# Kernel tuning notes

Measured on AMD Instinct MI355X. Metric: run time of the kernel, lower is better.

The kernel has to match this reference:

```python
import jax, jax.numpy as jnp
import numpy as np

H = 8          # query heads
HKV = 4        # kv heads
D = 256        # head dim
GROUPS = H // HKV
HIDDEN = 2304
WINDOW = 2048  # sliding window
SOFTCAP = 50.0
SCALE = (HIDDEN // H) ** -0.5  # query_pre_attn_scalar uses hidden//heads, not head_dim
NEG = -1e9
ROPE_BASE = 10000.0


def _rope_tables(L, offset=0, dtype=jnp.float32):
    inv_freq = 1.0 / (ROPE_BASE ** (jnp.arange(0, D, 2, dtype=jnp.float32) / D))
    t = jnp.arange(offset, offset + L, dtype=jnp.float32)
    freqs = jnp.outer(t, inv_freq)                    # [L, D/2]
    emb = jnp.concatenate([freqs, freqs], axis=-1)    # [L, D]
    return jnp.cos(emb).astype(dtype), jnp.sin(emb).astype(dtype)


def _rotate_half(x):
    x1, x2 = jnp.split(x, 2, axis=-1)
    return jnp.concatenate([-x2, x1], axis=-1)


def _apply_rope(x, cos, sin):
    # x: [B, h, L, D]; cos/sin: [L, D]
    return x * cos[None, None] + _rotate_half(x) * sin[None, None]


def setup_inputs() -> dict:
    key = jax.random.key(0)
    ks = jax.random.split(key, 5)
    B, L = 1, 4096
    x = jax.random.normal(ks[0], (B, L, HIDDEN), dtype=jnp.float32)
    wq = jax.random.normal(ks[1], (HIDDEN, H * D), dtype=jnp.float32) * 0.02
    wk = jax.random.normal(ks[2], (HIDDEN, HKV * D), dtype=jnp.float32) * 0.02
    wv = jax.random.normal(ks[3], (HIDDEN, HKV * D), dtype=jnp.float32) * 0.02
    wo = jax.random.normal(ks[4], (H * D, HIDDEN), dtype=jnp.float32) * 0.02
    # additive causal mask [1,1,L,L]
    causal = jnp.triu(jnp.full((L, L), NEG, dtype=jnp.float32), k=1)
    mask = causal[None, None]
    return {"x": x, "mask": mask, "wq": wq, "wk": wk, "wv": wv, "wo": wo}


def reference(x, mask, wq, wk, wv, wo):
    B, L, _ = x.shape
    q = (x @ wq).reshape(B, L, H, D).transpose(0, 2, 1, 3)     # [B,H,L,D]
    k = (x @ wk).reshape(B, L, HKV, D).transpose(0, 2, 1, 3)   # [B,HKV,L,D]
    v = (x @ wv).reshape(B, L, HKV, D).transpose(0, 2, 1, 3)

    cos, sin = _rope_tables(L, 0, q.dtype)
    q = _apply_rope(q, cos, sin)
    k = _apply_rope(k, cos, sin)

    # GQA: repeat_interleave kv heads
    k = jnp.repeat(k, GROUPS, axis=1)  # [B,H,L,D]
    v = jnp.repeat(v, GROUPS, axis=1)

    attn = jnp.einsum("bhqd,bhkd->bhqk", q, k) * SCALE
    attn = SOFTCAP * jnp.tanh(attn / SOFTCAP)
    attn = attn + mask

    kv_len = attn.shape[-1]
    if kv_len > WINDOW:  # sliding branch: keep only last WINDOW key columns
        col_keep = jnp.arange(kv_len) >= (kv_len - WINDOW)  # [kv_len]
        attn = jnp.where(col_keep[None, None, None, :], attn, NEG)

    attn = jax.nn.softmax(attn.astype(jnp.float32), axis=-1).astype(q.dtype)
    out = jnp.einsum("bhqk,bhkd->bhqd", attn, v)
    out = out.transpose(0, 2, 1, 3).reshape(B, L, H * D)
    return out @ wo
```

## Files before the change

kernel.cpp:

```cpp
#include <hip/hip_runtime.h>

typedef unsigned short u16;
typedef __bf16 bf16x8 __attribute__((ext_vector_type(8)));
typedef float floatx4 __attribute__((ext_vector_type(4)));
typedef unsigned short u16x4 __attribute__((ext_vector_type(4)));
typedef unsigned short u16x8 __attribute__((ext_vector_type(8)));

#define L_SEQ 4096
#define HID   2304
#define NH    8
#define NKV   4
#define HD    256
#define QDIM  2048
#define KVDIM 1024
#define SCALE_F 0.05892556509887896f

__device__ __forceinline__ u16 f2bf(float f) {
  unsigned u = __float_as_uint(f);
  u += 0x7FFFu + ((u >> 16) & 1u);
  return (u16)(u >> 16);
}
__device__ __forceinline__ float bf2f(u16 h) {
  return __uint_as_float(((unsigned)h) << 16);
}

__device__ __forceinline__ void async_load16(const u16* g, u16* lds_base) {
  __builtin_amdgcn_global_load_lds(
      (const __attribute__((address_space(1))) unsigned int*)g,
      (__attribute__((address_space(3))) unsigned int*)lds_base, 16, 0, 0);
}

__device__ __forceinline__ int swz(int m) { return (m + (m >> 2)) & 3; }

__global__ __launch_bounds__(256)
void cast_kernel(const float* __restrict__ in, u16* __restrict__ out, int n4) {
  int i = blockIdx.x * 256 + threadIdx.x;
  if (i < n4) {
    float4 v = *reinterpret_cast<const float4*>(&in[(size_t)i * 4]);
    u16x4 o;
    o[0] = f2bf(v.x); o[1] = f2bf(v.y); o[2] = f2bf(v.z); o[3] = f2bf(v.w);
    *reinterpret_cast<u16x4*>(&out[(size_t)i * 4]) = o;
  }
}

__global__ __launch_bounds__(256)
void transpose_kernel(const float* __restrict__ wq, const float* __restrict__ wk,
                      const float* __restrict__ wv, const float* __restrict__ wo,
                      u16* __restrict__ wqkvT, u16* __restrict__ woT) {
  const int z = blockIdx.z;
  const float* W; u16* WT; int K, N;
  if (z == 0)      { W = wq; WT = wqkvT;                            K = HID;  N = QDIM; }
  else if (z == 1) { W = wk; WT = wqkvT + (size_t)QDIM * HID;       K = HID;  N = KVDIM; }
  else if (z == 2) { W = wv; WT = wqkvT + (size_t)(QDIM + KVDIM) * HID; K = HID; N = KVDIM; }
  else             { W = wo; WT = woT;                              K = QDIM; N = HID; }
  const int n0 = blockIdx.x * 32, k0 = blockIdx.y * 32;
  if (n0 >= N || k0 >= K) return;
  __shared__ u16 t[32][33];
  const int c = threadIdx.x & 31, r4 = (threadIdx.x >> 5) * 4;
#pragma unroll
  for (int i = 0; i < 4; ++i)
    t[r4 + i][c] = f2bf(W[(size_t)(k0 + r4 + i) * N + n0 + c]);
  __syncthreads();
#pragma unroll
  for (int i = 0; i < 4; ++i)
    WT[(size_t)(n0 + r4 + i) * K + k0 + c] = t[c][r4 + i];
}

#define G256_NT 36

#define G256_BARRIER() __builtin_amdgcn_s_barrier()

#define G256_STAGE(bb, X, kh, tt)                                              \
  {                                                                            \
    const u16* g = (X) ? BT + (size_t)(n0 + w * 32 + srow) * HID               \
                       : A + (size_t)(m0 + w * 32 + srow) * HID;               \
    const int kc = (tt) * 64 + (kh) * 32 + schk;                               \
    async_load16(g + kc, &lds[bb][X][kh][(w * 32) * 32]);                      \
    async_load16(g + 16 * HID + kc, &lds[bb][X][kh][(w * 32 + 16) * 32]);      \
  }

#define G256_READS(bb, kk, ch)                                                 \
  {                                                                            \
    const u16* Ak = &lds[bb][0][kk][0];                                        \
    const u16* Bk = &lds[bb][1][kk][0];                                        \
    _Pragma("unroll") for (int mt = 0; mt < 4; ++mt)                           \
        af[mt] = *reinterpret_cast<const bf16x8*>(                             \
            &Ak[(wm + ((ch) * 4 + mt) * 16 + l16) * 32 + rsw]);                \
    _Pragma("unroll") for (int nt = 0; nt < 4; ++nt)                           \
        bfr[nt] = *reinterpret_cast<const bf16x8*>(                            \
            &Bk[(wn + nt * 16 + l16) * 32 + rsw]);                             \
  }

#define G256_MFMA(ch)                                                          \
  {                                                                            \
    __builtin_amdgcn_s_setprio(1);                                             \
    _Pragma("unroll") for (int mt = 0; mt < 4; ++mt)                           \
        _Pragma("unroll") for (int nt = 0; nt < 4; ++nt)                       \
            acc[(ch) * 4 + mt][nt] = __builtin_amdgcn_mfma_f32_16x16x32_bf16(  \
                af[mt], bfr[nt], acc[(ch) * 4 + mt][nt], 0, 0, 0);             \
    __builtin_amdgcn_s_setprio(0);                                             \
  }

#define G256_VMCNT4() __asm__ volatile("s_waitcnt vmcnt(4)")
#define G256_VMCNT0() __asm__ volatile("s_waitcnt vmcnt(0)")

__global__ __launch_bounds__(512)
void gemm256_kernel(const u16* __restrict__ A, const u16* __restrict__ BT,
                    u16* __restrict__ C) {
  __shared__ __align__(16) u16 lds[2][2][2][256 * 32];

  const int tid  = threadIdx.x;
  const int lane = tid & 63;
  const int w    = tid >> 6;
  const int l16  = lane & 15;
  const int quad = lane >> 4;
  const int wm   = (w >> 2) * 128;
  const int wn   = (w & 3) * 64;

  const int srow = lane >> 2;
  const int schk = (((lane & 3) ^ ((lane >> 3) & 3))) * 8;
  const int rsw = ((quad ^ ((l16 >> 1) & 3))) * 8;

  const int bid = blockIdx.x;
  const int id  = (bid & 7) * 20 + (bid >> 3);

  int m0, n0, region;
  if (id < 64)      { region = 0; n0 = (id & 7) * 256;          m0 = 2048 + (id >> 3) * 256; }
  else if (id < 96) { region = 1; const int i = id - 64;
                      n0 = 2048 + (i & 3) * 256;                m0 = 2048 + (i >> 2) * 256; }
  else              { region = 2; const int i = id - 96;
                      n0 = 3072 + (i & 3) * 256;                m0 = (i >> 2) * 256; }

  floatx4 acc[8][4];
#pragma unroll
  for (int i = 0; i < 8; ++i)
#pragma unroll
    for (int j = 0; j < 4; ++j) acc[i][j] = (floatx4){0.f, 0.f, 0.f, 0.f};

  G256_STAGE(0, 0, 0, 0); G256_STAGE(0, 1, 0, 0);
  G256_STAGE(0, 0, 1, 0); G256_STAGE(0, 1, 1, 0);
  G256_STAGE(1, 0, 0, 1); G256_STAGE(1, 1, 0, 1);
  G256_VMCNT4();
  G256_BARRIER();

#pragma unroll 2
  for (int t = 0; t < G256_NT; ++t) {
    const int bb = t & 1;
    bf16x8 af[4], bfr[4];

    G256_READS(bb, 0, 0);
    if (t + 1 < G256_NT) { G256_STAGE(bb ^ 1, 0, 1, t + 1); }
    G256_BARRIER();
    G256_MFMA(0);
    G256_BARRIER();

    G256_READS(bb, 0, 1);
    if (t + 1 < G256_NT) { G256_STAGE(bb ^ 1, 1, 1, t + 1); }
    G256_BARRIER();
    G256_MFMA(1);
    G256_BARRIER();

    G256_READS(bb, 1, 0);
    if (t + 2 < G256_NT) { G256_STAGE(bb, 0, 0, t + 2); }
    G256_BARRIER();
    G256_MFMA(0);
    G256_BARRIER();

    G256_READS(bb, 1, 1);
    if (t + 2 < G256_NT) { G256_STAGE(bb, 1, 0, t + 2); }
    G256_BARRIER();
    G256_MFMA(1);
    if (t < G256_NT - 2) { G256_VMCNT4(); }
    else                 { G256_VMCNT0(); }
    G256_BARRIER();
  }

#pragma unroll
  for (int mt = 0; mt < 8; ++mt)
#pragma unroll
    for (int nt = 0; nt < 4; ++nt) {
      const int mbase = m0 + wm + mt * 16 + quad * 4;
      const int n = n0 + wn + nt * 16 + l16;
      if (region == 0) {
        const size_t base = (size_t)(n >> 8) * L_SEQ * HD + (n & 255);
#pragma unroll
        for (int r = 0; r < 4; ++r)
          C[base + (size_t)(mbase + r) * HD] = f2bf(acc[mt][nt][r]);
      } else if (region == 1) {
        const int nk2 = n - QDIM;
        const size_t base = (size_t)NH * L_SEQ * HD +
                            (size_t)(nk2 >> 8) * L_SEQ * HD + (nk2 & 255);
#pragma unroll
        for (int r = 0; r < 4; ++r)
          C[base + (size_t)(mbase + r) * HD] = f2bf(acc[mt][nt][r]);
      } else {
        const int nv = n - QDIM - KVDIM;
        u16x4 o;
#pragma unroll
        for (int r = 0; r < 4; ++r) o[r] = f2bf(acc[mt][nt][r]);
        *reinterpret_cast<u16x4*>(
            &C[(size_t)(NH + NKV) * L_SEQ * HD +
               ((size_t)(nv >> 8) * HD + (nv & 255)) * L_SEQ + mbase]) = o;
      }
    }
}

template<int MODE>
__global__ __launch_bounds__(256)
void gemm_kernel(const u16* __restrict__ A, const u16* __restrict__ BT,
                 void* __restrict__ Cp, int N, int K) {
  __shared__ __align__(16) u16 Alds[128][32];
  __shared__ __align__(16) u16 Blds[128][32];

  const int tid  = threadIdx.x;
  const int lane = tid & 63;
  const int w    = tid >> 6;
  const int wm   = (w >> 1) * 64;
  const int wn   = (w & 1) * 64;
  const int l16  = lane & 15;
  const int quad = lane >> 4;

  int m0, n0;
  if (MODE == 0) {
    const int id = blockIdx.x;
    if (id < 256)      { n0 = (id & 15) * 128;                 m0 = 2048 + (id >> 4) * 128; }
    else if (id < 384) { const int i2 = id - 256;
                         n0 = 2048 + (i2 & 7) * 128;           m0 = 2048 + (i2 >> 3) * 128; }
    else               { const int i3 = id - 384;
                         n0 = 3072 + (i3 & 7) * 128;           m0 = (i3 >> 3) * 128; }
  } else {
    m0 = blockIdx.y * 128;
    n0 = blockIdx.x * 128;
  }

  const int srow_in = lane >> 2;
  const int schunk  = lane & 3;

  floatx4 acc[4][4];
#pragma unroll
  for (int i = 0; i < 4; ++i)
#pragma unroll
    for (int j = 0; j < 4; ++j) acc[i][j] = (floatx4){0.f, 0.f, 0.f, 0.f};

  const int nk = K >> 5;
  for (int kt = 0; kt < nk; ++kt) {
    __syncthreads();
#pragma unroll
    for (int p = 0; p < 2; ++p) {
      const int row = w * 32 + p * 16 + srow_in;
      const int ce  = schunk ^ swz(row);
      async_load16(&A[(size_t)(m0 + row) * K + kt * 32 + ce * 8], &Alds[w * 32 + p * 16][0]);
      async_load16(&BT[(size_t)(n0 + row) * K + kt * 32 + ce * 8], &Blds[w * 32 + p * 16][0]);
    }
    __syncthreads();

    bf16x8 a[4], b[4];
#pragma unroll
    for (int mt = 0; mt < 4; ++mt) {
      const int row = wm + mt * 16 + l16;
      a[mt] = *reinterpret_cast<const bf16x8*>(&Alds[row][(quad ^ swz(row)) * 8]);
    }
#pragma unroll
    for (int nt = 0; nt < 4; ++nt) {
      const int row = wn + nt * 16 + l16;
      b[nt] = *reinterpret_cast<const bf16x8*>(&Blds[row][(quad ^ swz(row)) * 8]);
    }
#pragma unroll
    for (int mt = 0; mt < 4; ++mt)
#pragma unroll
      for (int nt = 0; nt < 4; ++nt)
        acc[mt][nt] = __builtin_amdgcn_mfma_f32_16x16x32_bf16(a[mt], b[nt], acc[mt][nt], 0, 0, 0);
  }

#pragma unroll
  for (int mt = 0; mt < 4; ++mt)
#pragma unroll
    for (int nt = 0; nt < 4; ++nt) {
      const int mbase = m0 + wm + mt * 16 + quad * 4;
      const int n = n0 + wn + nt * 16 + l16;
      if (MODE == 0) {
        u16* C = (u16*)Cp;
        if (n < QDIM) {
          const size_t base = (size_t)(n >> 8) * L_SEQ * HD + (n & 255);
#pragma unroll
          for (int r = 0; r < 4; ++r)
            C[base + (size_t)(mbase + r) * HD] = f2bf(acc[mt][nt][r]);
        } else if (n < QDIM + KVDIM) {
          const int nk2 = n - QDIM;
          const size_t base = (size_t)NH * L_SEQ * HD +
                              (size_t)(nk2 >> 8) * L_SEQ * HD + (nk2 & 255);
#pragma unroll
          for (int r = 0; r < 4; ++r)
            C[base + (size_t)(mbase + r) * HD] = f2bf(acc[mt][nt][r]);
        } else {
          const int nv = n - QDIM - KVDIM;
          u16x4 o;
#pragma unroll
          for (int r = 0; r < 4; ++r) o[r] = f2bf(acc[mt][nt][r]);
          *reinterpret_cast<u16x4*>(
              &C[(size_t)(NH + NKV) * L_SEQ * HD +
                 ((size_t)(nv >> 8) * HD + (nv & 255)) * L_SEQ + mbase]) = o;
        }
      } else {
        float* C = (float*)Cp;
#pragma unroll
        for (int r = 0; r < 4; ++r)
          C[(size_t)(mbase + r) * N + n] = acc[mt][nt][r];
      }
    }
}

__global__ __launch_bounds__(128)
void rope_kernel(u16* __restrict__ qb, u16* __restrict__ kb) {
  const int l  = 2048 + blockIdx.x;
  const int hh = blockIdx.y;
  u16* base = (hh < NH) ? qb + ((size_t)hh * L_SEQ + l) * HD
                        : kb + ((size_t)(hh - NH) * L_SEQ + l) * HD;
  const int d = threadIdx.x;
  const float invf = exp2f((float)d * (-13.287712379549449f / 128.0f));
  const float ang = (float)l * invf;
  float s, c;
  sincosf(ang, &s, &c);
  const float x1 = bf2f(base[d]);
  const float x2 = bf2f(base[d + 128]);
  base[d]       = f2bf(x1 * c - x2 * s);
  base[d + 128] = f2bf(x2 * c + x1 * s);
}

__global__ __launch_bounds__(256)
void meanv_kernel(const u16* __restrict__ vt, float* __restrict__ mv) {
  const int row  = blockIdx.x * 4 + (threadIdx.x >> 6);
  const int lane = threadIdx.x & 63;
  const u16* p = vt + (size_t)row * L_SEQ;
  float s = 0.f;
#pragma unroll
  for (int c = 0; c < 8; ++c) {
    u16x8 v = *reinterpret_cast<const u16x8*>(&p[(c * 64 + lane) * 8]);
#pragma unroll
    for (int j = 0; j < 8; ++j) s += bf2f(v[j]);
  }
#pragma unroll
  for (int off = 32; off > 0; off >>= 1) s += __shfl_xor(s, off, 64);
  if (lane == 0) mv[row] = s * (1.0f / 4096.0f);
}

__global__ __launch_bounds__(256)
void rowvec_part_kernel(const float* __restrict__ mv, const float* __restrict__ wo,
                        float* __restrict__ rpart) {
  const int j = blockIdx.x * 256 + threadIdx.x;
  const int c0 = blockIdx.y * 128;
  float acc = 0.f;
#pragma unroll 4
  for (int cc = 0; cc < 128; ++cc) {
    const int c = c0 + cc;
    const float a = mv[((c >> 9) << 8) | (c & 255)];
    acc += a * wo[(size_t)c * HID + j];
  }
  rpart[blockIdx.y * HID + j] = acc;
}

__global__ __launch_bounds__(256)
void rowvec_reduce_kernel(const float* __restrict__ rpart, float* __restrict__ r) {
  const int j = blockIdx.x * 256 + threadIdx.x;
  float s = 0.f;
#pragma unroll
  for (int p = 0; p < 16; ++p) s += rpart[p * HID + j];
  r[j] = s;
}

__global__ __launch_bounds__(256)
void bcast_out_kernel(const float* __restrict__ r, float* __restrict__ out) {
  const int idx = blockIdx.x * 256 + threadIdx.x;
  const int col4 = idx % 576;
  *reinterpret_cast<float4*>(&out[(size_t)idx * 4]) =
      *reinterpret_cast<const float4*>(&r[col4 * 4]);
}

__global__ __launch_bounds__(256)
void attn_kernel(const u16* __restrict__ qb, const u16* __restrict__ kb,
                 const u16* __restrict__ vt, float* __restrict__ Opart,
                 float* __restrict__ lpart) {
  const int s = blockIdx.x;
  const int pr = blockIdx.y;
  const int h = blockIdx.z;
  const int kvh = h >> 1;
  const int tid = threadIdx.x;
  const int w = tid >> 6, lane = tid & 63;
  const int l16 = lane & 15, quad = lane >> 4;

  __shared__ __align__(16) u16 Klds[32 * 256];
  __shared__ __align__(16) u16 Vlds[256 * 32];
  __shared__ u16 Plds[4][16][40];

  const int n_a = 2 * pr + 2;
  const int lo = (66 * s) >> 2;
  const int hi = (66 * (s + 1)) >> 2;

  const int r_lo[2] = {lo, (lo > n_a) ? lo : n_a};
  const int r_hi[2] = {(hi < n_a) ? hi : n_a, hi};
  const int r_t[2]  = {32 + pr, 63 - pr};
  const int r_off[2] = {64, 64 - n_a};

  const u16* kg0 = kb + (size_t)kvh * L_SEQ * HD;
  const u16* vg0 = vt + (size_t)kvh * HD * L_SEQ;

  for (int run = 0; run < 2; ++run) {
    if (r_lo[run] >= r_hi[run]) continue;
    const int t  = r_t[run];
    const int q0 = t * 64 + w * 16;

    bf16x8 aq[8];
    {
      const u16* qr = qb + ((size_t)h * L_SEQ + q0 + l16) * HD + quad * 8;
#pragma unroll
      for (int f = 0; f < 8; ++f)
        aq[f] = *reinterpret_cast<const bf16x8*>(&qr[f * 32]);
    }

    floatx4 acc[16];
#pragma unroll
    for (int i = 0; i < 16; ++i) acc[i] = (floatx4){0.f, 0.f, 0.f, 0.f};
    float lsum[4] = {0.f, 0.f, 0.f, 0.f};

    for (int g = r_lo[run]; g < r_hi[run]; ++g) {
      const int kt = r_off[run] + g;
      __syncthreads();
      {
        const u16* kg = kg0 + (size_t)kt * 32 * HD;
#pragma unroll
        for (int p = 0; p < 4; ++p) {
          const int r   = w * 8 + p * 2 + (lane >> 5);
          const int pos = lane & 31;
          const int c   = (pos & 24) | ((pos ^ r) & 7);
          async_load16(&kg[(size_t)r * HD + c * 8], &Klds[(w * 8 + p * 2) * 256]);
        }
        const u16* vg = vg0 + kt * 32;
#pragma unroll
        for (int j = 0; j < 4; ++j) {
          const int m  = w * 32 + j * 8 + (lane >> 3);
          const int p  = lane & 7;
          const int c2 = p ^ (m & 7);
          const int r  = m * 2 + (c2 >> 2);
          async_load16(&vg[(size_t)r * L_SEQ + (c2 & 3) * 8], &Vlds[(w * 32 + j * 8) * 64]);
        }
      }
      __syncthreads();

      floatx4 sa[2] = {(floatx4){0.f, 0.f, 0.f, 0.f}, (floatx4){0.f, 0.f, 0.f, 0.f}};
#pragma unroll
      for (int nt = 0; nt < 2; ++nt) {
        const int row = nt * 16 + l16;
#pragma unroll
        for (int f = 0; f < 8; ++f) {
          const int c   = f * 4 + quad;
          const int pos = (c & 24) | ((c ^ row) & 7);
          bf16x8 bk = *reinterpret_cast<const bf16x8*>(&Klds[row * 256 + pos * 8]);
          sa[nt] = __builtin_amdgcn_mfma_f32_16x16x32_bf16(aq[f], bk, sa[nt], 0, 0, 0);
        }
      }
#pragma unroll
      for (int nt = 0; nt < 2; ++nt) {
        const int key = kt * 32 + nt * 16 + l16;
#pragma unroll
        for (int r = 0; r < 4; ++r) {
          const float x = sa[nt][r] * SCALE_F;
          const float capm50 = -100.0f / (__expf(x * 0.04f) + 1.0f);
          float p = __expf(capm50);
          const int qq = q0 + quad * 4 + r;
          p = (key <= qq) ? p : 0.0f;
          lsum[r] += p;
          Plds[w][quad * 4 + r][nt * 16 + l16] = f2bf(p);
        }
      }
      __asm__ volatile("s_waitcnt lgkmcnt(0)" ::: "memory");
      bf16x8 ap = *reinterpret_cast<const bf16x8*>(&Plds[w][l16][quad * 8]);
#pragma unroll
      for (int dt = 0; dt < 16; ++dt) {
        const int rV = dt * 16 + l16;
        const int m  = rV >> 1;
        const int p  = ((rV & 1) * 4 + quad) ^ (m & 7);
        bf16x8 bv = *reinterpret_cast<const bf16x8*>(&Vlds[m * 64 + p * 8]);
        acc[dt] = __builtin_amdgcn_mfma_f32_16x16x32_bf16(ap, bv, acc[dt], 0, 0, 0);
      }
    }

#pragma unroll
    for (int r = 0; r < 4; ++r) {
      float l = lsum[r];
      l += __shfl_xor(l, 1); l += __shfl_xor(l, 2);
      l += __shfl_xor(l, 4); l += __shfl_xor(l, 8);
      lsum[r] = l;
    }
    const int ql0 = q0 - 2048 + quad * 4;
#pragma unroll
    for (int r = 0; r < 4; ++r) {
      float* orow = Opart + (((size_t)s * NH + h) * 2048 + ql0 + r) * HD + l16;
#pragma unroll
      for (int dt = 0; dt < 16; ++dt) orow[dt * 16] = acc[dt][r];
      if (l16 == 0) lpart[((size_t)s * NH + h) * 2048 + ql0 + r] = lsum[r];
    }
  }
}

__global__ __launch_bounds__(256)
void combine_kernel(const float* __restrict__ Opart, const float* __restrict__ lpart,
                    u16* __restrict__ ab) {
  const int idx4 = blockIdx.x * 256 + threadIdx.x;
  const int d4 = (idx4 & 63) * 4;
  const int ql = (idx4 >> 6) & 2047;
  const int h  = idx4 >> 17;
  const int qtile = ql >> 6;
  const bool role_a = qtile < 16;
  const int pr = role_a ? qtile : 31 - qtile;
  const int lo_s[4] = {0, 16, 33, 49};
  const int hi_s[4] = {16, 33, 49, 66};

  float4 o = {0.f, 0.f, 0.f, 0.f};
  float l = 0.f;
#pragma unroll
  for (int s = 0; s < 4; ++s) {
    const bool valid = role_a ? (lo_s[s] < 2 * pr + 2) : (hi_s[s] > 2 * pr + 2);
    if (valid) {
      float4 v = *reinterpret_cast<const float4*>(
          &Opart[(((size_t)s * NH + h) * 2048 + ql) * HD + d4]);
      o.x += v.x; o.y += v.y; o.z += v.z; o.w += v.w;
      l += lpart[((size_t)s * NH + h) * 2048 + ql];
    }
  }
  const float inv = 1.0f / l;
  u16x4 ov;
  ov[0] = f2bf(o.x * inv); ov[1] = f2bf(o.y * inv);
  ov[2] = f2bf(o.z * inv); ov[3] = f2bf(o.w * inv);
  *reinterpret_cast<u16x4*>(&ab[(size_t)(2048 + ql) * QDIM + h * HD + d4]) = ov;
}

extern "C" void kernel_launch(void* const* d_in, const int* in_sizes, int n_in,
                              void* d_out, int out_size, void* d_ws, size_t ws_size,
                              hipStream_t stream) {
  const float* x  = (const float*)d_in[0];
  const float* wq = (const float*)d_in[2];
  const float* wk = (const float*)d_in[3];
  const float* wv = (const float*)d_in[4];
  const float* wo = (const float*)d_in[5];
  float* out = (float*)d_out;

  u16* qb  = (u16*)d_ws;
  u16* kb  = qb  + (size_t)NH  * L_SEQ * HD;
  u16* vtb = kb  + (size_t)NKV * L_SEQ * HD;
  u16* ab  = vtb + (size_t)NKV * L_SEQ * HD;
  u16* xb  = ab  + (size_t)L_SEQ * QDIM;
  u16* wqkvT = xb + (size_t)L_SEQ * HID;
  u16* woT = wqkvT + (size_t)(QDIM + 2 * KVDIM) * HID;
  float* Opart = (float*)(woT + (size_t)HID * QDIM);
  float* lpart = Opart + (size_t)4 * NH * 2048 * HD;
  float* mv    = lpart + (size_t)4 * NH * 2048;
  float* rpart = mv + 1024;
  float* rvec  = rpart + 16 * HID;

  cast_kernel<<<dim3(L_SEQ * HID / 4 / 256), 256, 0, stream>>>(x, xb, L_SEQ * HID / 4);
  transpose_kernel<<<dim3(72, 72, 4), 256, 0, stream>>>(wq, wk, wv, wo, wqkvT, woT);

  gemm256_kernel<<<dim3(160), 512, 0, stream>>>(xb, wqkvT, qb);
  rope_kernel<<<dim3(L_SEQ / 2, NH + NKV), 128, 0, stream>>>(qb, kb);
  meanv_kernel<<<dim3(256), 256, 0, stream>>>(vtb, mv);

  rowvec_part_kernel<<<dim3(9, 16), 256, 0, stream>>>(mv, wo, rpart);
  rowvec_reduce_kernel<<<dim3(9), 256, 0, stream>>>(rpart, rvec);
  bcast_out_kernel<<<dim3(2048 * 576 / 256), 256, 0, stream>>>(rvec, out);

  attn_kernel<<<dim3(4, 16, NH), 256, 0, stream>>>(qb, kb, vtb, Opart, lpart);
  combine_kernel<<<dim3(4096), 256, 0, stream>>>(Opart, lpart, ab);

  gemm_kernel<1><<<dim3(HID / 128, 2048 / 128), 256, 0, stream>>>(
      ab + (size_t)2048 * QDIM, woT, out + (size_t)2048 * HID, HID, QDIM);
}
```

Before: 376.3 us.

## Prefetch LDS fragments ahead and halve barriers in gemm256 main loop

Restructures the gemm256 inner loop so A and B fragments are read from LDS one sub-step ahead into separate register sets. B fragments are reused across both M halves instead of being reloaded. Barriers drop from eight to four per iteration, and sched_barrier pins the read, async-load and MFMA ordering. This aims to overlap LDS reads with MFMA and cut synchronisation stalls, at the cost of more live vector registers. There is also a risk of LDS overwrite races, since the async stages now issue with fewer barriers around them.

```diff
diff --git a/kernel.cpp b/kernel.cpp
--- a/kernel.cpp
+++ b/kernel.cpp
@@ -69,6 +69,7 @@
 #define G256_NT 36
 
 #define G256_BARRIER() __builtin_amdgcn_s_barrier()
+#define G256_SCHEDB()  __builtin_amdgcn_sched_barrier(0)
 
 #define G256_STAGE(bb, X, kh, tt)                                              \
   {                                                                            \
@@ -79,25 +80,29 @@
     async_load16(g + 16 * HID + kc, &lds[bb][X][kh][(w * 32 + 16) * 32]);      \
   }
 
-#define G256_READS(bb, kk, ch)                                                 \
+#define G256_RD_B(dst, bb, kk)                                                 \
+  {                                                                            \
+    const u16* Bk = &lds[bb][1][kk][0];                                        \
+    _Pragma("unroll") for (int nt = 0; nt < 4; ++nt)                           \
+        dst[nt] = *reinterpret_cast<const bf16x8*>(                            \
+            &Bk[(wn + nt * 16 + l16) * 32 + rsw]);                             \
+  }
+
+#define G256_RD_A(dst, bb, kk, ch)                                             \
   {                                                                            \
     const u16* Ak = &lds[bb][0][kk][0];                                        \
-    const u16* Bk = &lds[bb][1][kk][0];                                        \
     _Pragma("unroll") for (int mt = 0; mt < 4; ++mt)                           \
-        af[mt] = *reinterpret_cast<const bf16x8*>(                             \
+        dst[mt] = *reinterpret_cast<const bf16x8*>(                            \
             &Ak[(wm + ((ch) * 4 + mt) * 16 + l16) * 32 + rsw]);                \
-    _Pragma("unroll") for (int nt = 0; nt < 4; ++nt)                           \
-        bfr[nt] = *reinterpret_cast<const bf16x8*>(                            \
-            &Bk[(wn + nt * 16 + l16) * 32 + rsw]);                             \
-  }
-
-#define G256_MFMA(ch)                                                          \
+  }
+
+#define G256_MFMA(ch, AA, BB)                                                  \
   {                                                                            \
     __builtin_amdgcn_s_setprio(1);                                             \
     _Pragma("unroll") for (int mt = 0; mt < 4; ++mt)                           \
         _Pragma("unroll") for (int nt = 0; nt < 4; ++nt)                       \
             acc[(ch) * 4 + mt][nt] = __builtin_amdgcn_mfma_f32_16x16x32_bf16(  \
-                af[mt], bfr[nt], acc[(ch) * 4 + mt][nt], 0, 0, 0);             \
+                AA[mt], BB[nt], acc[(ch) * 4 + mt][nt], 0, 0, 0);              \
     __builtin_amdgcn_s_setprio(0);                                             \
   }
 
@@ -146,30 +151,32 @@
 #pragma unroll 2
   for (int t = 0; t < G256_NT; ++t) {
     const int bb = t & 1;
-    bf16x8 af[4], bfr[4];
-
-    G256_READS(bb, 0, 0);
+    bf16x8 a_cur[4], b_cur[4], a_hi0[4], a_lo1[4], b1[4], a_hi1[4];
+
+    G256_RD_A(a_cur, bb, 0, 0);
+    G256_RD_B(b_cur, bb, 0);
+    G256_RD_A(a_hi0, bb, 0, 1);
     if (t + 1 < G256_NT) { G256_STAGE(bb ^ 1, 0, 1, t + 1); }
+    G256_SCHEDB();
+    G256_MFMA(0, a_cur, b_cur);
     G256_BARRIER();
-    G256_MFMA(0);
+
+    G256_RD_A(a_lo1, bb, 1, 0);
+    G256_RD_B(b1, bb, 1);
+    if (t + 1 < G256_NT) { G256_STAGE(bb ^ 1, 1, 1, t + 1); }
+    G256_SCHEDB();
+    G256_MFMA(1, a_hi0, b_cur);
     G256_BARRIER();
 
-    G256_READS(bb, 0, 1);
-    if (t + 1 < G256_NT) { G256_STAGE(bb ^ 1, 1, 1, t + 1); }
+    G256_RD_A(a_hi1, bb, 1, 1);
+    if (t + 2 < G256_NT) { G256_STAGE(bb, 0, 0, t + 2); }
+    G256_SCHEDB();
+    G256_MFMA(0, a_lo1, b1);
     G256_BARRIER();
-    G256_MFMA(1);
-    G256_BARRIER();
-
-    G256_READS(bb, 1, 0);
-    if (t + 2 < G256_NT) { G256_STAGE(bb, 0, 0, t + 2); }
-    G256_BARRIER();
-    G256_MFMA(0);
-    G256_BARRIER();
-
-    G256_READS(bb, 1, 1);
+
     if (t + 2 < G256_NT) { G256_STAGE(bb, 1, 0, t + 2); }
-    G256_BARRIER();
-    G256_MFMA(1);
+    G256_SCHEDB();
+    G256_MFMA(1, a_hi1, b1);
     if (t < G256_NT - 2) { G256_VMCNT4(); }
     else                 { G256_VMCNT0(); }
     G256_BARRIER();
```

Result: faster. 368.2 us (-2.1%).
